# Kernel tuning notes

Hardware: AMD Instinct MI355X
Metric: run time of the kernel (lower is better)

The kernel has to match this reference:

```python
import jax, jax.numpy as jnp
import numpy as np
from jax import lax

BLANK = 27
NEG = -1e30  # safe -inf substitute (avoids NaN grads through logaddexp)


def _joint_log_probs(enc, dec, We, Wd, bf, Wp, bp):
    # Concat-then-Linear == sum of per-branch matmuls: [e;d] @ Wf = e@We + d@Wd.
    f = jnp.einsum('bte,eh->bth', enc, We)          # [B,T,H]
    g = jnp.einsum('bud,dh->buh', dec, Wd)          # [B,U1,H]
    h = jnp.tanh(f[:, :, None, :] + g[:, None, :, :] + bf)  # [B,T,U1,H]
    logits = jnp.einsum('btuh,hv->btuv', h, Wp) + bp         # [B,T,U1,V]
    return jax.nn.log_softmax(logits, axis=-1)


def _rnnt_loss_one(lp, tgt, t_len, u_len):
    # lp: [T,U1,V] log-probs, tgt: [U] int labels, t_len/u_len: scalars.
    T, U1, V = lp.shape
    blank_lp = lp[:, :, BLANK]                                   # [T,U1]
    lab_lp = jnp.take_along_axis(lp[:, :U1 - 1, :],
                                 tgt[None, :, None], axis=2)[..., 0]  # [T,U]

    # alpha[0,:] : only label emissions along u at t=0.
    alpha0 = jnp.concatenate([jnp.zeros((1,), lp.dtype),
                              jnp.cumsum(lab_lp[0])])            # [U1]

    def step(prev_alpha, inp):
        b_prev, lab_t = inp                       # [U1], [U]
        from_below = prev_alpha + b_prev          # blank move from t-1
        first = from_below[0]

        def inner(carry, x):
            fb, lab = x
            new = jnp.logaddexp(fb, carry + lab)  # blank-from-below vs label-from-left
            return new, new

        _, rest = lax.scan(inner, first, (from_below[1:], lab_t))
        alpha_t = jnp.concatenate([first[None], rest])
        return alpha_t, alpha_t

    _, alphas = lax.scan(step, alpha0, (blank_lp[:-1], lab_lp[1:]))
    alpha = jnp.concatenate([alpha0[None], alphas], axis=0)      # [T,U1]

    # Terminal: emit final blank at (t_len-1, u_len).
    return -(alpha[t_len - 1, u_len] + blank_lp[t_len - 1, u_len])


def setup_inputs() -> dict:
    key = jax.random.key(0)
    ks = jax.random.split(key, 10)
    B, T, U, E, D, H, V = 8, 400, 60, 256, 256, 512, 28
    enc_state = jax.random.normal(ks[0], (B, T, E), jnp.float32)
    dec_state = jax.random.normal(ks[1], (B, U + 1, D), jnp.float32)
    targets = jax.random.randint(ks[2], (B, U), 0, BLANK, jnp.int32)
    inputs_length = jax.random.randint(ks[3], (B,), 200, T + 1, jnp.int32)
    targets_length = jax.random.randint(ks[4], (B,), 30, U + 1, jnp.int32)
    s1 = 1.0 / np.sqrt(E + D)
    s2 = 1.0 / np.sqrt(H)
    We = jax.random.normal(ks[5], (E, H), jnp.float32) * s1
    Wd = jax.random.normal(ks[6], (D, H), jnp.float32) * s1
    bf = jax.random.normal(ks[7], (H,), jnp.float32) * s1
    Wp = jax.random.normal(ks[8], (H, V), jnp.float32) * s2
    bp = jax.random.normal(ks[9], (V,), jnp.float32) * s2
    return {"enc_state": enc_state, "dec_state": dec_state,
            "We": We, "Wd": Wd, "bf": bf, "Wp": Wp, "bp": bp,
            "targets": targets, "inputs_length": inputs_length,
            "targets_length": targets_length}


def reference(enc_state, dec_state, We, Wd, bf, Wp, bp,
              targets, inputs_length, targets_length):
    lp = _joint_log_probs(enc_state, dec_state, We, Wd, bf, Wp, bp)
    loss = jax.vmap(_rnnt_loss_one)(lp, targets, inputs_length, targets_length)
    return loss  # [B], reduction='none'
```

## Files before the change

kernel.cpp:

```cpp
#include <hip/hip_runtime.h>
#include <hip/hip_bf16.h>
#include <math.h>

#define NEGF (-1e30f)
#define LOG2E 1.4426950408889634f
#define TSCALE 2.885390081777927f

typedef __attribute__((ext_vector_type(8))) short bf16x8;
typedef __attribute__((ext_vector_type(4))) float f32x4;

#define DROWS_PAD 480
#define DPITCH 64
#define PF 16

__device__ __forceinline__ unsigned short f2bf(float x) {
    __hip_bfloat16 h = __float2bfloat16(x);
    return *reinterpret_cast<unsigned short*>(&h);
}

__device__ __forceinline__ float wave_shr1(float x) {
    int i = __builtin_bit_cast(int, x);
    int r = __builtin_amdgcn_update_dpp(0, i, 0x138, 0xf, 0xf, true);
    return __builtin_bit_cast(float, r);
}

__device__ __forceinline__ float4 rcp4_nr(float4 d) {
    float4 y;
    y.x = __builtin_bit_cast(float, 0x7EF311C3 - __builtin_bit_cast(int, d.x));
    y.y = __builtin_bit_cast(float, 0x7EF311C3 - __builtin_bit_cast(int, d.y));
    y.z = __builtin_bit_cast(float, 0x7EF311C3 - __builtin_bit_cast(int, d.z));
    y.w = __builtin_bit_cast(float, 0x7EF311C3 - __builtin_bit_cast(int, d.w));
    float4 t;
    t.x = fmaf(-d.x, y.x, 2.f); t.y = fmaf(-d.y, y.y, 2.f);
    t.z = fmaf(-d.z, y.z, 2.f); t.w = fmaf(-d.w, y.w, 2.f);
    y.x *= t.x; y.y *= t.y; y.z *= t.z; y.w *= t.w;
    return y;
}

__global__ __launch_bounds__(256) void k_pack(const float* __restrict__ We,
                                              const float* __restrict__ Wd,
                                              const float* __restrict__ Wp,
                                              const float* __restrict__ bp,
                                              unsigned short* __restrict__ WeFrag,
                                              unsigned short* __restrict__ WdFrag,
                                              unsigned short* __restrict__ BfragP,
                                              float* __restrict__ csbp) {
    int gid = blockIdx.x * 256 + threadIdx.x;
    if (gid < 32768) {
        const float* W = (gid < 16384) ? We : Wd;
        unsigned short* F = (gid < 16384) ? WeFrag : WdFrag;
        int s = gid & 16383;
        int lane = s & 63;
        int c = (s >> 6) & 7;
        int nt = s >> 9;
        int n = nt * 16 + (lane & 15);
        int kbase = c * 32 + ((lane >> 4) & 3) * 8;
        unsigned short* dst = F + (size_t)s * 8;
#pragma unroll
        for (int j = 0; j < 8; ++j) dst[j] = f2bf(W[(size_t)(kbase + j) * 512 + n]);
    } else if (gid < 34816) {
        int s = gid - 32768;
        int lane = s & 63;
        int half = (s >> 6) & 1;
        int c = s >> 7;
        int n = half * 16 + (lane & 15);
        int kbase = c * 32 + (lane >> 4) * 8;
        unsigned short* dst = BfragP + (size_t)s * 8;
#pragma unroll
        for (int j = 0; j < 8; ++j) {
            float v = (n < 28) ? (-2.f * Wp[(kbase + j) * 28 + n]) : 0.f;
            dst[j] = f2bf(v);
        }
    } else if (gid < 34848) {
        int v = gid - 34816;
        float s = 0.f;
        if (v < 28) {
            for (int k = 0; k < 512; ++k) s += Wp[k * 28 + v];
            s += bp[v];
        }
        csbp[v] = s;
    }
}

__global__ __launch_bounds__(256) void k_gemm(const float* __restrict__ enc,
                                              const float* __restrict__ dec,
                                              const float* __restrict__ bfv,
                                              const unsigned short* __restrict__ WeFrag,
                                              const unsigned short* __restrict__ WdFrag,
                                              float* __restrict__ f,
                                              float* __restrict__ g) {
    const int wid = blockIdx.x * 4 + threadIdx.y;
    const int lane = threadIdx.x;
    const int m16 = lane & 15;
    const int quad = lane >> 4;

    const float* A; const unsigned short* WF; float* Out; int M, rt, ct; bool isg;
    if (wid < 1600) { A = enc; WF = WeFrag; Out = f; M = 3200; rt = wid >> 3; ct = wid & 7; isg = false; }
    else { int w2 = wid - 1600; A = dec; WF = WdFrag; Out = g; M = 488; rt = w2 >> 3; ct = w2 & 7; isg = true; }

    const int row = rt * 16 + m16;
    const float* arow = A + (size_t)min(row, M - 1) * 256 + quad * 8;

    f32x4 acc[4];
#pragma unroll
    for (int i = 0; i < 4; ++i) acc[i] = (f32x4){0.f, 0.f, 0.f, 0.f};

#pragma unroll
    for (int c = 0; c < 8; ++c) {
        float4 a0 = *(const float4*)(arow + c * 32);
        float4 a1 = *(const float4*)(arow + c * 32 + 4);
        union { unsigned short s[8]; bf16x8 v; } Af;
        Af.s[0] = f2bf(a0.x); Af.s[1] = f2bf(a0.y);
        Af.s[2] = f2bf(a0.z); Af.s[3] = f2bf(a0.w);
        Af.s[4] = f2bf(a1.x); Af.s[5] = f2bf(a1.y);
        Af.s[6] = f2bf(a1.z); Af.s[7] = f2bf(a1.w);
#pragma unroll
        for (int i = 0; i < 4; ++i) {
            int nt = ct * 4 + i;
            bf16x8 Bv = *(const bf16x8*)(WF + (size_t)((nt * 8 + c) * 64 + lane) * 8);
            acc[i] = __builtin_amdgcn_mfma_f32_16x16x32_bf16(Af.v, Bv, acc[i], 0, 0, 0);
        }
    }

#pragma unroll
    for (int i = 0; i < 4; ++i) {
        int n = ct * 64 + i * 16 + m16;
        float bv = isg ? bfv[n] : 0.f;
#pragma unroll
        for (int r = 0; r < 4; ++r) {
            int ro = rt * 16 + quad * 4 + r;
            if (ro < M) Out[(size_t)ro * 512 + n] = (acc[i][r] + bv) * TSCALE;
        }
    }
}

__global__ __launch_bounds__(256) void k_cells(const float* __restrict__ f,
                                               const float* __restrict__ g,
                                               const unsigned short* __restrict__ Bfrag,
                                               const float* __restrict__ csbp,
                                               const int* __restrict__ targets,
                                               const int* __restrict__ ilen,
                                               const int* __restrict__ ulenp,
                                               float2* __restrict__ pairD) {
    const int b = blockIdx.z;
    const int tlen = ilen[b];
    const int t0 = blockIdx.x * 16;
    if (t0 >= tlen) return;
    if ((int)blockIdx.y * 4 > ulenp[b]) return;
    const int wave = threadIdx.y;
    const int lane = threadIdx.x;
    const int u_raw = blockIdx.y * 4 + wave;
    const int u = min(u_raw, 60);
    const int tid = wave * 64 + lane;

    __shared__ float fs[16 * 516];

    {
        const float4* src = (const float4*)(f + (size_t)(b * 400 + t0) * 512);
#pragma unroll
        for (int i = 0; i < 8; ++i) {
            int idx = tid + i * 256;
            int row = idx >> 7;
            int c4 = idx & 127;
            float4 v = src[idx];
            *(float4*)&fs[row * 516 + c4 * 4] = v;
        }
    }
    __syncthreads();

    const int quad = lane >> 4;
    const int m16 = lane & 15;
    const float* gu = g + (size_t)(b * 61 + u) * 512 + quad * 8;
    const float* fsrow = fs + m16 * 516 + quad * 8;
    f32x4 acc0 = {0.f, 0.f, 0.f, 0.f};
    f32x4 acc1 = {0.f, 0.f, 0.f, 0.f};
    const float4 one4 = make_float4(1.f, 1.f, 1.f, 1.f);

#pragma unroll 4
    for (int c = 0; c < 16; ++c) {
        float4 fa = *(const float4*)(fsrow + c * 32);
        float4 fb = *(const float4*)(fsrow + c * 32 + 4);
        float4 ga = *(const float4*)(gu + c * 32);
        float4 gb = *(const float4*)(gu + c * 32 + 4);
        float4 s0 = fa + ga;
        float4 s1 = fb + gb;
        float4 e0, e1;
        e0.x = __builtin_amdgcn_exp2f(s0.x); e0.y = __builtin_amdgcn_exp2f(s0.y);
        e0.z = __builtin_amdgcn_exp2f(s0.z); e0.w = __builtin_amdgcn_exp2f(s0.w);
        e1.x = __builtin_amdgcn_exp2f(s1.x); e1.y = __builtin_amdgcn_exp2f(s1.y);
        e1.z = __builtin_amdgcn_exp2f(s1.z); e1.w = __builtin_amdgcn_exp2f(s1.w);
        float4 r0 = rcp4_nr(e0 + one4);
        float4 r1 = rcp4_nr(e1 + one4);
        union { unsigned short s[8]; bf16x8 v; } A;
        A.s[0] = f2bf(r0.x); A.s[1] = f2bf(r0.y);
        A.s[2] = f2bf(r0.z); A.s[3] = f2bf(r0.w);
        A.s[4] = f2bf(r1.x); A.s[5] = f2bf(r1.y);
        A.s[6] = f2bf(r1.z); A.s[7] = f2bf(r1.w);
        bf16x8 B0 = *(const bf16x8*)(Bfrag + ((size_t)(c * 2 + 0) * 64 + lane) * 8);
        bf16x8 B1 = *(const bf16x8*)(Bfrag + ((size_t)(c * 2 + 1) * 64 + lane) * 8);
        acc0 = __builtin_amdgcn_mfma_f32_16x16x32_bf16(A.v, B0, acc0, 0, 0, 0);
        acc1 = __builtin_amdgcn_mfma_f32_16x16x32_bf16(A.v, B1, acc1, 0, 0, 0);
    }

    float cs0 = csbp[m16];
    int n1 = 16 + m16;
    bool n1v = (n1 < 28);
    float cs1 = csbp[n1 & 31];
    int tv = targets[b * 60 + min(u, 59)];

    float res_blank[4], res_lab[4];
#pragma unroll
    for (int r = 0; r < 4; ++r) {
        float l0 = acc0[r] + cs0;
        float l1 = n1v ? (acc1[r] + cs1) : NEGF;
        float mx = fmaxf(l0, l1);
        mx = fmaxf(mx, __shfl_xor(mx, 1, 64));
        mx = fmaxf(mx, __shfl_xor(mx, 2, 64));
        mx = fmaxf(mx, __shfl_xor(mx, 4, 64));
        mx = fmaxf(mx, __shfl_xor(mx, 8, 64));
        float s = __builtin_amdgcn_exp2f((l0 - mx) * LOG2E) +
                  __builtin_amdgcn_exp2f((l1 - mx) * LOG2E);
        s += __shfl_xor(s, 1, 64);
        s += __shfl_xor(s, 2, 64);
        s += __shfl_xor(s, 4, 64);
        s += __shfl_xor(s, 8, 64);
        float lse = mx + __logf(s);
        int base = lane & 48;
        float labsrc = (tv < 16) ? l0 : l1;
        float labv = __shfl(labsrc, base | (tv & 15), 64);
        float blankv = __shfl(l1, base | 11, 64);
        res_blank[r] = blankv - lse;
        res_lab[r] = labv - lse;
    }

    if (m16 == 0 && u_raw <= 60) {
        float2* Pd = pairD + (size_t)b * (DROWS_PAD * DPITCH);
#pragma unroll
        for (int r = 0; r < 4; ++r) {
            int t = t0 + quad * 4 + r;
            if (t < tlen) {
                int d = t + u;
                float2 pr;
                pr.x = res_blank[r];
                pr.y = (u <= 59) ? res_lab[r] : NEGF;
                Pd[d * DPITCH + u] = pr;
            }
        }
    }
}

__global__ __launch_bounds__(64) void k_alpha(const float2* __restrict__ pairD,
                                              const int* __restrict__ ilen,
                                              const int* __restrict__ ulenp,
                                              float* __restrict__ out) {
    const int b = blockIdx.x;
    const int u = threadIdx.x;
    const float2* Pd = pairD + (size_t)b * (DROWS_PAD * DPITCH);
    const int tl = ilen[b];
    const int ul = ulenp[b];
    const int dstar = tl - 1 + ul;
    const int dmax = ((dstar + PF - 1) / PF) * PF;
    const bool uok = (u <= 60);
    const bool lok = (u >= 1 && u <= 60);

    float cur = (u == 0) ? 0.f : NEGF;
    float saved = NEGF;

    float2 pf[PF];
#pragma unroll
    for (int i = 0; i < PF; ++i) pf[i] = Pd[i * DPITCH + u];

    for (int d0 = 1; d0 <= dmax; d0 += PF) {
#pragma unroll
        for (int i = 0; i < PF; ++i) {
            const int d = d0 + i;
            float2 v = pf[i];
            pf[i] = Pd[(d + PF - 1) * DPITCH + u];
            int t = d - u;
            float bv = (t >= 1 && t <= 399 && uok) ? v.x : NEGF;
            float lvn = wave_shr1(v.y);
            float lv = (lok && t >= 0 && t <= 399) ? lvn : NEGF;
            float up = wave_shr1(cur);
            float a = cur + bv;
            float c2 = up + lv;
            float mx = fmaxf(a, c2), mn = fminf(a, c2);
            float nv = mx + __logf(1.f + __builtin_amdgcn_exp2f((mn - mx) * LOG2E));
            bool valid = (t >= 0 && t <= 399 && uok);
            cur = valid ? nv : cur;
            saved = (d == dstar) ? cur : saved;
        }
    }
    if (u == ul) out[b] = -(saved + Pd[dstar * DPITCH + u].x);
}

extern "C" void kernel_launch(void* const* d_in, const int* in_sizes, int n_in,
                              void* d_out, int out_size, void* d_ws, size_t ws_size,
                              hipStream_t stream) {
    const float* enc = (const float*)d_in[0];
    const float* dec = (const float*)d_in[1];
    const float* We  = (const float*)d_in[2];
    const float* Wd  = (const float*)d_in[3];
    const float* bf  = (const float*)d_in[4];
    const float* Wp  = (const float*)d_in[5];
    const float* bp  = (const float*)d_in[6];
    const int* targets = (const int*)d_in[7];
    const int* ilen    = (const int*)d_in[8];
    const int* ulen    = (const int*)d_in[9];
    float* out = (float*)d_out;
    float* ws = (float*)d_ws;

    float* f     = ws;
    float* g     = ws + 1638400;
    unsigned short* BfragP = (unsigned short*)(ws + 1888256);
    unsigned short* WeFrag = (unsigned short*)(ws + 1896448);
    unsigned short* WdFrag = (unsigned short*)(ws + 1961984);
    float* csbp  = ws + 2027520;
    float2* pairD = (float2*)(ws + 2027552);

    k_pack<<<137, 256, 0, stream>>>(We, Wd, Wp, bp, WeFrag, WdFrag, BfragP, csbp);

    k_gemm<<<462, dim3(64, 4, 1), 0, stream>>>(enc, dec, bf, WeFrag, WdFrag, f, g);

    dim3 gridC(25, 16, 8);
    dim3 blockC(64, 4, 1);
    k_cells<<<gridC, blockC, 0, stream>>>(f, g, BfragP, csbp, targets, ilen, ulen, pairD);

    k_alpha<<<8, 64, 0, stream>>>(pairD, ilen, ulen, out);
}
```

Before: 158.1 us.

## Fuse alpha recursion into cells kernel with per-chunk completion counters

Removes the separate alpha kernel. Eight extra blocks inside the cells grid run the diagonal alpha recursion per batch, spin-waiting on per-time-chunk atomic completion counters, so the recursion overlaps with log-prob cell computation and one launch is saved. Log-probs are now stored in base-2 units so the recursion can use log2/exp2 directly without rescaling multiplies. The change relies on co-residency of producer and consumer blocks (dispatch order), uses relaxed atomics without explicit acquire fences, and has a guard-bounded spin that could read stale data.

After: 169.2 us. 7.0% more time.

```diff
diff --git a/kernel.cpp b/kernel.cpp
--- a/kernel.cpp
+++ b/kernel.cpp
@@ -4,6 +4,7 @@
 
 #define NEGF (-1e30f)
 #define LOG2E 1.4426950408889634f
+#define LN2F 0.6931471805599453f
 #define TSCALE 2.885390081777927f
 
 typedef __attribute__((ext_vector_type(8))) short bf16x8;
@@ -12,6 +13,7 @@
 #define DROWS_PAD 480
 #define DPITCH 64
 #define PF 16
+#define NTCH 25
 
 __device__ __forceinline__ unsigned short f2bf(float x) {
     __hip_bfloat16 h = __float2bfloat16(x);
@@ -44,7 +46,8 @@
                                               unsigned short* __restrict__ WeFrag,
                                               unsigned short* __restrict__ WdFrag,
                                               unsigned short* __restrict__ BfragP,
-                                              float* __restrict__ csbp) {
+                                              float* __restrict__ csbp,
+                                              int* __restrict__ doneCnt) {
     int gid = blockIdx.x * 256 + threadIdx.x;
     if (gid < 32768) {
         const float* W = (gid < 16384) ? We : Wd;
@@ -79,6 +82,8 @@
             s += bp[v];
         }
         csbp[v] = s;
+    } else if (gid < 35104) {
+        doneCnt[gid - 34848] = 0;
     }
 }
 
@@ -141,8 +146,76 @@
                                                const int* __restrict__ targets,
                                                const int* __restrict__ ilen,
                                                const int* __restrict__ ulenp,
-                                               float2* __restrict__ pairD) {
+                                               float2* __restrict__ pairD,
+                                               int* __restrict__ doneCnt,
+                                               float* __restrict__ out) {
     const int b = blockIdx.z;
+
+    if (blockIdx.x == NTCH) {
+        if (blockIdx.y != 0 || threadIdx.y != 0) return;
+        const int u = threadIdx.x;
+        const float2* Pd = pairD + (size_t)b * (DROWS_PAD * DPITCH);
+        const int* dn = doneCnt + b * 32;
+        const int tl = ilen[b];
+        const int ul = ulenp[b];
+        const int nU = (ul >> 2) + 1;
+        const int tcLast = (tl - 1) >> 4;
+        const int dstar = tl - 1 + ul;
+        const int dmax = ((dstar + PF - 1) / PF) * PF;
+        const bool uok = (u <= 60);
+        const bool lok = (u >= 1 && u <= 60);
+
+        int tcCur = -1;
+        int nextCnt = __hip_atomic_load(dn, __ATOMIC_RELAXED, __HIP_MEMORY_SCOPE_AGENT);
+
+#define GATE(NEED) do {                                                          \
+            int need_ = (NEED); need_ = min(need_, tcLast);                      \
+            int guard_ = 0;                                                      \
+            while (tcCur < need_) {                                              \
+                if (nextCnt >= nU) { ++tcCur; }                                  \
+                else { __builtin_amdgcn_s_sleep(2);                              \
+                       if (++guard_ > (1 << 20)) break; }                        \
+                nextCnt = __hip_atomic_load(dn + min(tcCur + 1, tcLast),         \
+                              __ATOMIC_RELAXED, __HIP_MEMORY_SCOPE_AGENT);       \
+            }                                                                    \
+            asm volatile("" ::: "memory");                                       \
+        } while (0)
+
+        float cur = (u == 0) ? 0.f : NEGF;
+        float saved = NEGF, savedBlank = NEGF;
+
+        GATE((PF - 1) >> 4);
+        float2 pf[PF];
+#pragma unroll
+        for (int i = 0; i < PF; ++i) pf[i] = Pd[i * DPITCH + u];
+
+        for (int d0 = 1; d0 <= dmax; d0 += PF) {
+            GATE((d0 + 2 * PF - 2) >> 4);
+#pragma unroll
+            for (int i = 0; i < PF; ++i) {
+                const int d = d0 + i;
+                float2 v = pf[i];
+                pf[i] = Pd[(d + PF - 1) * DPITCH + u];
+                int t = d - u;
+                float bv = (t >= 1 && t <= 399 && uok) ? v.x : NEGF;
+                float lvn = wave_shr1(v.y);
+                float lv = (lok && t >= 0 && t <= 399) ? lvn : NEGF;
+                float up = wave_shr1(cur);
+                float a = cur + bv;
+                float c2 = up + lv;
+                float mx = fmaxf(a, c2), mn = fminf(a, c2);
+                float nv = mx + __log2f(1.f + __builtin_amdgcn_exp2f(mn - mx));
+                bool valid = (t >= 0 && t <= 399 && uok);
+                cur = valid ? nv : cur;
+                saved = (d == dstar) ? cur : saved;
+                savedBlank = (d == dstar) ? v.x : savedBlank;
+            }
+        }
+        if (u == ul) out[b] = -(saved + savedBlank) * LN2F;
+        return;
+#undef GATE
+    }
+
     const int tlen = ilen[b];
     const int t0 = blockIdx.x * 16;
     if (t0 >= tlen) return;
@@ -229,8 +302,8 @@
         float labsrc = (tv < 16) ? l0 : l1;
         float labv = __shfl(labsrc, base | (tv & 15), 64);
         float blankv = __shfl(l1, base | 11, 64);
-        res_blank[r] = blankv - lse;
-        res_lab[r] = labv - lse;
+        res_blank[r] = (blankv - lse) * LOG2E;
+        res_lab[r] = (labv - lse) * LOG2E;
     }
 
     if (m16 == 0 && u_raw <= 60) {
@@ -243,54 +316,18 @@
                 float2 pr;
                 pr.x = res_blank[r];
                 pr.y = (u <= 59) ? res_lab[r] : NEGF;
-                Pd[d * DPITCH + u] = pr;
+                __hip_atomic_store((unsigned long long*)&Pd[d * DPITCH + u],
+                                   __builtin_bit_cast(unsigned long long, pr),
+                                   __ATOMIC_RELAXED, __HIP_MEMORY_SCOPE_AGENT);
             }
         }
     }
-}
-
-__global__ __launch_bounds__(64) void k_alpha(const float2* __restrict__ pairD,
-                                              const int* __restrict__ ilen,
-                                              const int* __restrict__ ulenp,
-                                              float* __restrict__ out) {
-    const int b = blockIdx.x;
-    const int u = threadIdx.x;
-    const float2* Pd = pairD + (size_t)b * (DROWS_PAD * DPITCH);
-    const int tl = ilen[b];
-    const int ul = ulenp[b];
-    const int dstar = tl - 1 + ul;
-    const int dmax = ((dstar + PF - 1) / PF) * PF;
-    const bool uok = (u <= 60);
-    const bool lok = (u >= 1 && u <= 60);
-
-    float cur = (u == 0) ? 0.f : NEGF;
-    float saved = NEGF;
-
-    float2 pf[PF];
-#pragma unroll
-    for (int i = 0; i < PF; ++i) pf[i] = Pd[i * DPITCH + u];
-
-    for (int d0 = 1; d0 <= dmax; d0 += PF) {
-#pragma unroll
-        for (int i = 0; i < PF; ++i) {
-            const int d = d0 + i;
-            float2 v = pf[i];
-            pf[i] = Pd[(d + PF - 1) * DPITCH + u];
-            int t = d - u;
-            float bv = (t >= 1 && t <= 399 && uok) ? v.x : NEGF;
-            float lvn = wave_shr1(v.y);
-            float lv = (lok && t >= 0 && t <= 399) ? lvn : NEGF;
-            float up = wave_shr1(cur);
-            float a = cur + bv;
-            float c2 = up + lv;
-            float mx = fmaxf(a, c2), mn = fminf(a, c2);
-            float nv = mx + __logf(1.f + __builtin_amdgcn_exp2f((mn - mx) * LOG2E));
-            bool valid = (t >= 0 && t <= 399 && uok);
-            cur = valid ? nv : cur;
-            saved = (d == dstar) ? cur : saved;
-        }
-    }
-    if (u == ul) out[b] = -(saved + Pd[dstar * DPITCH + u].x);
+
+    __syncthreads();
+    if (tid == 0) {
+        __hip_atomic_fetch_add(doneCnt + b * 32 + blockIdx.x, 1,
+                               __ATOMIC_RELAXED, __HIP_MEMORY_SCOPE_AGENT);
+    }
 }
 
 extern "C" void kernel_launch(void* const* d_in, const int* in_sizes, int n_in,
@@ -316,14 +353,14 @@
     unsigned short* WdFrag = (unsigned short*)(ws + 1961984);
     float* csbp  = ws + 2027520;
     float2* pairD = (float2*)(ws + 2027552);
-
-    k_pack<<<137, 256, 0, stream>>>(We, Wd, Wp, bp, WeFrag, WdFrag, BfragP, csbp);
+    int* doneCnt = (int*)(ws + 2519072);
+
+    k_pack<<<138, 256, 0, stream>>>(We, Wd, Wp, bp, WeFrag, WdFrag, BfragP, csbp, doneCnt);
 
     k_gemm<<<462, dim3(64, 4, 1), 0, stream>>>(enc, dec, bf, WeFrag, WdFrag, f, g);
 
-    dim3 gridC(25, 16, 8);
+    dim3 gridC(NTCH + 1, 16, 8);
     dim3 blockC(64, 4, 1);
-    k_cells<<<gridC, blockC, 0, stream>>>(f, g, BfragP, csbp, targets, ilen, ulen, pairD);
-
-    k_alpha<<<8, 64, 0, stream>>>(pairD, ilen, ulen, out);
-}
+    k_cells<<<gridC, blockC, 0, stream>>>(f, g, BfragP, csbp, targets, ilen, ulen,
+                                          pairD, doneCnt, out);
+}
```

## Read f rows directly from global memory and run alpha recursion in log2 domain

Applied to the files above, without the earlier changes.

k_cells no longer stages the 16-row f tile in shared memory behind a __syncthreads. Each lane now loads its f row straight from global (L1/L2) memory, the unroll goes from 4 to 8, and launch bounds request 8 blocks per CU. k_alpha now works in base-2 log space: log-probs are pre-scaled by LOG2E, which drops a multiply per step, the final blank value is captured in a register instead of re-read, and the result is rescaled by ln2. The risk is more redundant global traffic, since the four waves share the same f rows, plus register pressure from the occupancy hint.

Measured after the change: 171.2 us. +8.3%, slower.

```diff
diff --git a/kernel.cpp b/kernel.cpp
--- a/kernel.cpp
+++ b/kernel.cpp
@@ -4,6 +4,7 @@
 
 #define NEGF (-1e30f)
 #define LOG2E 1.4426950408889634f
+#define LN2F 0.6931471805599453f
 #define TSCALE 2.885390081777927f
 
 typedef __attribute__((ext_vector_type(8))) short bf16x8;
@@ -134,14 +135,14 @@
     }
 }
 
-__global__ __launch_bounds__(256) void k_cells(const float* __restrict__ f,
-                                               const float* __restrict__ g,
-                                               const unsigned short* __restrict__ Bfrag,
-                                               const float* __restrict__ csbp,
-                                               const int* __restrict__ targets,
-                                               const int* __restrict__ ilen,
-                                               const int* __restrict__ ulenp,
-                                               float2* __restrict__ pairD) {
+__global__ __launch_bounds__(256, 8) void k_cells(const float* __restrict__ f,
+                                                  const float* __restrict__ g,
+                                                  const unsigned short* __restrict__ Bfrag,
+                                                  const float* __restrict__ csbp,
+                                                  const int* __restrict__ targets,
+                                                  const int* __restrict__ ilen,
+                                                  const int* __restrict__ ulenp,
+                                                  float2* __restrict__ pairD) {
     const int b = blockIdx.z;
     const int tlen = ilen[b];
     const int t0 = blockIdx.x * 16;
@@ -151,35 +152,19 @@
     const int lane = threadIdx.x;
     const int u_raw = blockIdx.y * 4 + wave;
     const int u = min(u_raw, 60);
-    const int tid = wave * 64 + lane;
-
-    __shared__ float fs[16 * 516];
-
-    {
-        const float4* src = (const float4*)(f + (size_t)(b * 400 + t0) * 512);
-#pragma unroll
-        for (int i = 0; i < 8; ++i) {
-            int idx = tid + i * 256;
-            int row = idx >> 7;
-            int c4 = idx & 127;
-            float4 v = src[idx];
-            *(float4*)&fs[row * 516 + c4 * 4] = v;
-        }
-    }
-    __syncthreads();
 
     const int quad = lane >> 4;
     const int m16 = lane & 15;
     const float* gu = g + (size_t)(b * 61 + u) * 512 + quad * 8;
-    const float* fsrow = fs + m16 * 516 + quad * 8;
+    const float* fr = f + (size_t)(b * 400 + t0 + m16) * 512 + quad * 8;
     f32x4 acc0 = {0.f, 0.f, 0.f, 0.f};
     f32x4 acc1 = {0.f, 0.f, 0.f, 0.f};
     const float4 one4 = make_float4(1.f, 1.f, 1.f, 1.f);
 
-#pragma unroll 4
+#pragma unroll 8
     for (int c = 0; c < 16; ++c) {
-        float4 fa = *(const float4*)(fsrow + c * 32);
-        float4 fb = *(const float4*)(fsrow + c * 32 + 4);
+        float4 fa = *(const float4*)(fr + c * 32);
+        float4 fb = *(const float4*)(fr + c * 32 + 4);
         float4 ga = *(const float4*)(gu + c * 32);
         float4 gb = *(const float4*)(gu + c * 32 + 4);
         float4 s0 = fa + ga;
@@ -229,8 +214,8 @@
         float labsrc = (tv < 16) ? l0 : l1;
         float labv = __shfl(labsrc, base | (tv & 15), 64);
         float blankv = __shfl(l1, base | 11, 64);
-        res_blank[r] = blankv - lse;
-        res_lab[r] = labv - lse;
+        res_blank[r] = (blankv - lse) * LOG2E;
+        res_lab[r] = (labv - lse) * LOG2E;
     }
 
     if (m16 == 0 && u_raw <= 60) {
@@ -264,7 +249,7 @@
     const bool lok = (u >= 1 && u <= 60);
 
     float cur = (u == 0) ? 0.f : NEGF;
-    float saved = NEGF;
+    float saved = NEGF, savedBlank = NEGF;
 
     float2 pf[PF];
 #pragma unroll
@@ -284,13 +269,14 @@
             float a = cur + bv;
             float c2 = up + lv;
             float mx = fmaxf(a, c2), mn = fminf(a, c2);
-            float nv = mx + __logf(1.f + __builtin_amdgcn_exp2f((mn - mx) * LOG2E));
+            float nv = mx + __log2f(1.f + __builtin_amdgcn_exp2f(mn - mx));
             bool valid = (t >= 0 && t <= 399 && uok);
             cur = valid ? nv : cur;
             saved = (d == dstar) ? cur : saved;
-        }
-    }
-    if (u == ul) out[b] = -(saved + Pd[dstar * DPITCH + u].x);
+            savedBlank = (d == dstar) ? v.x : savedBlank;
+        }
+    }
+    if (u == ul) out[b] = -(saved + savedBlank) * LN2F;
 }
 
 extern "C" void kernel_launch(void* const* d_in, const int* in_sizes, int n_in,
```
